# Kernel optimization log

Hardware: AMD Instinct MI355X
Metric: run time of the kernel (lower is better)

The kernel has to match this reference:

```python
import jax, jax.numpy as jnp
import numpy as np

N = 100000
E = 1600000
D_IN = 256
HID = 128
EPS = 1e-5


def setup_inputs() -> dict:
    key = jax.random.key(0)
    ks = jax.random.split(key, 8)
    x = jax.random.normal(ks[0], (N, D_IN), dtype=jnp.float32)
    edge_index = jax.random.randint(ks[1], (2, E), 0, N, dtype=jnp.int64)
    edge_weight = jax.random.uniform(ks[2], (E,), dtype=jnp.float32)
    # GCNConv lin weights (glorot-ish scale) + bias
    W1 = jax.random.normal(ks[3], (D_IN, HID), dtype=jnp.float32) / np.sqrt(D_IN)
    b1 = jnp.zeros((HID,), dtype=jnp.float32)
    W2 = jax.random.normal(ks[4], (HID, HID), dtype=jnp.float32) / np.sqrt(HID)
    b2 = jnp.zeros((HID,), dtype=jnp.float32)
    # BatchNorm affine params
    g1 = jnp.ones((HID,), dtype=jnp.float32)
    be1 = jnp.zeros((HID,), dtype=jnp.float32)
    g2 = jnp.ones((HID,), dtype=jnp.float32)
    be2 = jnp.zeros((HID,), dtype=jnp.float32)
    return {"x": x, "edge_index": edge_index, "edge_weight": edge_weight,
            "W1": W1, "b1": b1, "g1": g1, "be1": be1,
            "W2": W2, "b2": b2, "g2": g2, "be2": be2}


def _gcn_layer(h, src, dst, w, W, b):
    # GCNConv(add_self_loops=False, normalize=False):
    # h' = h @ W; out[i] = sum_{(j->i)} w_ji * h'[j]; out += b
    h = h @ W                                   # [N, out_dim]
    msg = w[:, None] * jnp.take(h, src, axis=0)  # [E, out_dim]
    agg = jax.ops.segment_sum(msg, dst, num_segments=N)
    return agg + b


def _bn(h, gamma, beta):
    # BatchNorm1d with batch statistics (biased variance), training-mode math
    mean = jnp.mean(h, axis=0)
    var = jnp.mean(jnp.square(h - mean), axis=0)
    return (h - mean) * jax.lax.rsqrt(var + EPS) * gamma + beta


def reference(x, edge_index, edge_weight, W1, b1, g1, be1, W2, b2, g2, be2):
    src = edge_index[0]
    dst = edge_index[1]
    h = _gcn_layer(x, src, dst, edge_weight, W1, b1)
    h = jax.nn.relu(_bn(h, g1, be1))
    h = _gcn_layer(h, src, dst, edge_weight, W2, b2)
    h = jax.nn.relu(_bn(h, g2, be2))  # last_activation=True
    return h
```

## Files before the change

### kernel.cpp

```cpp
#include <hip/hip_runtime.h>
#include <hip/hip_bf16.h>

#define NNODES 100000
#define DIN    256
#define NHID   128
#define EPS    1e-5f
#define SHIFT  9
#define NB2    ((NNODES + 511) >> SHIFT)
#define BCAP2  9216
#define CURPAD 16
#define PH     2048

typedef __attribute__((ext_vector_type(8))) short short8v;
typedef __attribute__((ext_vector_type(4))) float f32x4;

static __device__ __forceinline__ unsigned short f2bf(float v) {
    __hip_bfloat16 b = __float2bfloat16(v);
    return *reinterpret_cast<unsigned short*>(&b);
}
static __device__ __forceinline__ float bfhi2f(unsigned int u) {
    union { unsigned int i; float f; } x; x.i = u & 0xFFFF0000u; return x.f;
}
static __device__ __forceinline__ float bflo2f(unsigned int u) {
    union { unsigned int i; float f; } x; x.i = u << 16; return x.f;
}

__global__ __launch_bounds__(256) void wtrans2_kernel(const float* __restrict__ W1,
                                                      const float* __restrict__ W2,
                                                      unsigned short* __restrict__ Wt1,
                                                      unsigned short* __restrict__ Wt2) {
    int i = blockIdx.x * 256 + threadIdx.x;
    if (i < DIN * NHID) {
        const int k = i >> 7, c = i & 127;
        Wt1[c * DIN + k] = f2bf(W1[i]);
    } else {
        i -= DIN * NHID;
        if (i < NHID * NHID) {
            const int k = i >> 7, c = i & 127;
            Wt2[c * NHID + k] = f2bf(W2[i]);
        }
    }
}

template <int K, int MODE>
__global__ __launch_bounds__(256) void mfma_gemm(const float* __restrict__ Af,
                                                 const unsigned short* __restrict__ Wtb,
                                                 const float* __restrict__ SS,
                                                 unsigned short* __restrict__ C, int M) {
    constexpr int NS = K / 32;
    constexpr int PADB = 40;
    __shared__ unsigned short As[2][128 * PADB];
    __shared__ float ssl[256];

    const int t = threadIdx.x;
    if (MODE == 1) {
        ssl[t] = SS[t];
        __syncthreads();
    }

    const int wid = t >> 6;
    const int lane = t & 63;
    const int wr = wid >> 1, wc = wid & 1;
    const int l15 = lane & 15, g = lane >> 4;
    const int R0 = blockIdx.x * 128;
    const int RW = R0 + wr * 64;

    const int srow = t >> 3;
    const int scol = (t & 7) * 4;

    f32x4 acc[4][4] = {};

    auto STAGE = [&](int s, int buf) {
        const int k0 = s * 32;
#pragma unroll
        for (int i = 0; i < 4; ++i) {
            const int row = srow + i * 32;
            int grow = R0 + row;
            grow = grow < M ? grow : M - 1;
            float4 v = *reinterpret_cast<const float4*>(Af + (size_t)grow * K + k0 + scol);
            if (MODE == 1) {
                v.x = fmaxf(fmaf(v.x, ssl[k0 + scol],     ssl[128 + k0 + scol]),     0.f);
                v.y = fmaxf(fmaf(v.y, ssl[k0 + scol + 1], ssl[128 + k0 + scol + 1]), 0.f);
                v.z = fmaxf(fmaf(v.z, ssl[k0 + scol + 2], ssl[128 + k0 + scol + 2]), 0.f);
                v.w = fmaxf(fmaf(v.w, ssl[k0 + scol + 3], ssl[128 + k0 + scol + 3]), 0.f);
            }
            ushort4 bv;
            bv.x = f2bf(v.x); bv.y = f2bf(v.y); bv.z = f2bf(v.z); bv.w = f2bf(v.w);
            *reinterpret_cast<ushort4*>(&As[buf][row * PADB + scol]) = bv;
        }
    };

    STAGE(0, 0);
    __syncthreads();

    for (int s = 0; s < NS; ++s) {
        if (s + 1 < NS) STAGE(s + 1, (s + 1) & 1);
        const unsigned short* ab = As[s & 1];
        short8v b[4];
#pragma unroll
        for (int n = 0; n < 4; ++n) {
            const int col = wc * 64 + n * 16 + l15;
            b[n] = *reinterpret_cast<const short8v*>(&Wtb[(size_t)col * K + s * 32 + g * 8]);
        }
        short8v a[4];
#pragma unroll
        for (int m = 0; m < 4; ++m) {
            const int row = wr * 64 + m * 16 + l15;
            a[m] = *reinterpret_cast<const short8v*>(&ab[row * PADB + g * 8]);
        }
#pragma unroll
        for (int m = 0; m < 4; ++m)
#pragma unroll
            for (int n = 0; n < 4; ++n)
                acc[m][n] = __builtin_amdgcn_mfma_f32_16x16x32_bf16(a[m], b[n], acc[m][n], 0, 0, 0);
        __syncthreads();
    }

#pragma unroll
    for (int m = 0; m < 4; ++m) {
#pragma unroll
        for (int q = 0; q < 4; ++q) {
            const int row = RW + m * 16 + g * 4 + q;
            if (row < M) {
                unsigned short* cp = C + (size_t)row * NHID + wc * 64 + l15;
#pragma unroll
                for (int n = 0; n < 4; ++n)
                    cp[n * 16] = f2bf(acc[m][n][q]);
            }
        }
    }
}

__global__ __launch_bounds__(256) void part_kernel(const int* __restrict__ src,
                                                   const int* __restrict__ dst,
                                                   const float* __restrict__ w,
                                                   int* __restrict__ gcur,
                                                   int2* __restrict__ bstage, int E) {
    __shared__ int2 staged[PH];
    __shared__ unsigned char aux[PH];
    __shared__ int hist[NB2], scn[NB2], cur[NB2], gbase[NB2];
    __shared__ int part[256];

    const int t = threadIdx.x;
    const int nchunk = (E + PH - 1) / PH;
    for (int c = blockIdx.x; c < nchunk; c += gridDim.x) {
        const int e0 = c * PH;
        const int cnt = min(PH, E - e0);
        for (int i = t; i < NB2; i += 256) hist[i] = 0;
        __syncthreads();

        int2 pay[8];
        int bk[8];
#pragma unroll
        for (int j = 0; j < 8; ++j) {
            const int i = j * 256 + t;
            bk[j] = -1;
            if (i < cnt) {
                const int e = e0 + i;
                const int d = dst[e];
                bk[j] = d >> SHIFT;
                pay[j].x = src[e] | ((d & 511) << 17);
                pay[j].y = __float_as_int(w[e]);
                atomicAdd(&hist[bk[j]], 1);
            }
        }
        __syncthreads();

        part[t] = (t < NB2) ? hist[t] : 0;
        __syncthreads();
        for (int off = 1; off < 256; off <<= 1) {
            const int v = (t >= off) ? part[t - off] : 0;
            __syncthreads();
            part[t] += v;
            __syncthreads();
        }
        if (t < NB2) {
            const int ex = part[t] - hist[t];
            scn[t] = ex;
            cur[t] = ex;
        }
        __syncthreads();

#pragma unroll
        for (int j = 0; j < 8; ++j) {
            if (bk[j] >= 0) {
                const int p = atomicAdd(&cur[bk[j]], 1);
                staged[p] = pay[j];
                aux[p] = (unsigned char)bk[j];
            }
        }
        if (t < NB2 && hist[t] > 0) gbase[t] = atomicAdd(&gcur[t * CURPAD], hist[t]);
        __syncthreads();

        for (int i = t; i < cnt; i += 256) {
            const int b = aux[i];
            const int p = gbase[b] + (i - scn[b]);
            if (p < BCAP2) bstage[(size_t)b * BCAP2 + p] = staged[i];
        }
        __syncthreads();
    }
}

__global__ __launch_bounds__(256) void csr_kernel(const int* __restrict__ gcur,
                                                  const int2* __restrict__ bstage,
                                                  int2* __restrict__ row_be,
                                                  int2* __restrict__ s_iw) {
    const int b = blockIdx.x;
    const int t = threadIdx.x;
    int cnt = gcur[b * CURPAD];
    if (cnt > BCAP2) cnt = BCAP2;
    const int sbase = b * BCAP2;

    __shared__ int hist[512], cur[512];
    __shared__ int part[256];
    for (int i = t; i < 512; i += 256) hist[i] = 0;
    __syncthreads();
    for (int i = t; i < cnt; i += 256)
        atomicAdd(&hist[(bstage[sbase + i].x >> 17) & 511], 1);
    __syncthreads();

    int loc[2];
    loc[0] = hist[t * 2];
    loc[1] = hist[t * 2 + 1];
    const int s0 = loc[0] + loc[1];
    part[t] = s0;
    __syncthreads();
    for (int off = 1; off < 256; off <<= 1) {
        const int v = (t >= off) ? part[t - off] : 0;
        __syncthreads();
        part[t] += v;
        __syncthreads();
    }
    int run = part[t] - s0;
#pragma unroll
    for (int j = 0; j < 2; ++j) {
        const int lb = t * 2 + j;
        cur[lb] = run;
        const int d = (b << SHIFT) + lb;
        if (d < NNODES) {
            int2 be;
            be.x = sbase + run;
            be.y = sbase + run + loc[j];
            row_be[d] = be;
        }
        run += loc[j];
    }
    __syncthreads();

    for (int i = t; i < cnt; i += 256) {
        const int2 e = bstage[sbase + i];
        const int l = (e.x >> 17) & 511;
        const int p = atomicAdd(&cur[l], 1);
        int2 o;
        o.x = e.x & 0x1FFFF;
        o.y = e.y;
        s_iw[sbase + p] = o;
    }
}

__global__ __launch_bounds__(256) void aggregate_kernel(const unsigned short* __restrict__ hb,
                                                        const int2* __restrict__ row_be,
                                                        const int2* __restrict__ s_iw,
                                                        float* __restrict__ out, int n) {
    const int wid = (blockIdx.x * 256 + threadIdx.x) >> 6;
    if (wid >= n) return;
    const int lane = threadIdx.x & 63;
    const int grp = lane >> 4;
    const int l16 = lane & 15;
    const int2 be = row_be[wid];
    const int end = be.y;

    float acc[8] = {};
    int j = be.x + grp;
    for (; j + 4 < end; j += 8) {
        const int2 e0 = s_iw[j];
        const int2 e1 = s_iw[j + 4];
        const uint4 v0 = *reinterpret_cast<const uint4*>(hb + (size_t)e0.x * NHID + l16 * 8);
        const uint4 v1 = *reinterpret_cast<const uint4*>(hb + (size_t)e1.x * NHID + l16 * 8);
        const float w0 = __int_as_float(e0.y);
        const float w1 = __int_as_float(e1.y);
        acc[0] = fmaf(w0, bflo2f(v0.x), acc[0]); acc[1] = fmaf(w0, bfhi2f(v0.x), acc[1]);
        acc[2] = fmaf(w0, bflo2f(v0.y), acc[2]); acc[3] = fmaf(w0, bfhi2f(v0.y), acc[3]);
        acc[4] = fmaf(w0, bflo2f(v0.z), acc[4]); acc[5] = fmaf(w0, bfhi2f(v0.z), acc[5]);
        acc[6] = fmaf(w0, bflo2f(v0.w), acc[6]); acc[7] = fmaf(w0, bfhi2f(v0.w), acc[7]);
        acc[0] = fmaf(w1, bflo2f(v1.x), acc[0]); acc[1] = fmaf(w1, bfhi2f(v1.x), acc[1]);
        acc[2] = fmaf(w1, bflo2f(v1.y), acc[2]); acc[3] = fmaf(w1, bfhi2f(v1.y), acc[3]);
        acc[4] = fmaf(w1, bflo2f(v1.z), acc[4]); acc[5] = fmaf(w1, bfhi2f(v1.z), acc[5]);
        acc[6] = fmaf(w1, bflo2f(v1.w), acc[6]); acc[7] = fmaf(w1, bfhi2f(v1.w), acc[7]);
    }
    if (j < end) {
        const int2 e0 = s_iw[j];
        const uint4 v0 = *reinterpret_cast<const uint4*>(hb + (size_t)e0.x * NHID + l16 * 8);
        const float w0 = __int_as_float(e0.y);
        acc[0] = fmaf(w0, bflo2f(v0.x), acc[0]); acc[1] = fmaf(w0, bfhi2f(v0.x), acc[1]);
        acc[2] = fmaf(w0, bflo2f(v0.y), acc[2]); acc[3] = fmaf(w0, bfhi2f(v0.y), acc[3]);
        acc[4] = fmaf(w0, bflo2f(v0.z), acc[4]); acc[5] = fmaf(w0, bfhi2f(v0.z), acc[5]);
        acc[6] = fmaf(w0, bflo2f(v0.w), acc[6]); acc[7] = fmaf(w0, bfhi2f(v0.w), acc[7]);
    }
#pragma unroll
    for (int k = 0; k < 8; ++k) {
        acc[k] += __shfl_xor(acc[k], 16, 64);
        acc[k] += __shfl_xor(acc[k], 32, 64);
    }
    if (grp == 0) {
        float4 a, b;
        a.x = acc[0]; a.y = acc[1]; a.z = acc[2]; a.w = acc[3];
        b.x = acc[4]; b.y = acc[5]; b.z = acc[6]; b.w = acc[7];
        float4* op = reinterpret_cast<float4*>(out + (size_t)wid * NHID + l16 * 8);
        op[0] = a;
        op[1] = b;
    }
}

__global__ __launch_bounds__(256) void stats_kernel(const float* __restrict__ h,
                                                    float* __restrict__ sums, int nrows) {
    const int col = threadIdx.x & 127;
    const int half = threadIdx.x >> 7;
    float s = 0.f, sq = 0.f;
    for (int r = blockIdx.x * 2 + half; r < nrows; r += gridDim.x * 2) {
        const float v = h[(size_t)r * NHID + col];
        s += v;
        sq += v * v;
    }
    __shared__ float ls[256], lq[256];
    ls[threadIdx.x] = s;
    lq[threadIdx.x] = sq;
    __syncthreads();
    if (threadIdx.x < 128) {
        atomicAdd(&sums[col], ls[threadIdx.x] + ls[threadIdx.x + 128]);
        atomicAdd(&sums[128 + col], lq[threadIdx.x] + lq[threadIdx.x + 128]);
    }
}

__global__ void finalize_kernel(const float* __restrict__ sums,
                                const float* __restrict__ gamma,
                                const float* __restrict__ beta,
                                float* __restrict__ ss) {
    const int c = threadIdx.x;
    const float invN = 1.0f / (float)NNODES;
    const float mean = sums[c] * invN;
    const float var = sums[128 + c] * invN - mean * mean;
    const float scale = gamma[c] * rsqrtf(var + EPS);
    ss[c] = scale;
    ss[128 + c] = beta[c] - mean * scale;
}

__global__ __launch_bounds__(256) void apply_f32_kernel(const float* __restrict__ in,
                                                        const float* __restrict__ ss,
                                                        float* __restrict__ out, int n4) {
    const int idx = blockIdx.x * 256 + threadIdx.x;
    if (idx >= n4) return;
    const int c = (idx & 31) * 4;
    const float4 v = reinterpret_cast<const float4*>(in)[idx];
    const float4 sc = *reinterpret_cast<const float4*>(ss + c);
    const float4 sh = *reinterpret_cast<const float4*>(ss + 128 + c);
    float4 r;
    r.x = fmaxf(fmaf(v.x, sc.x, sh.x), 0.f);
    r.y = fmaxf(fmaf(v.y, sc.y, sh.y), 0.f);
    r.z = fmaxf(fmaf(v.z, sc.z, sh.z), 0.f);
    r.w = fmaxf(fmaf(v.w, sc.w, sh.w), 0.f);
    reinterpret_cast<float4*>(out)[idx] = r;
}

extern "C" void kernel_launch(void* const* d_in, const int* in_sizes, int n_in,
                              void* d_out, int out_size, void* d_ws, size_t ws_size,
                              hipStream_t stream) {
    const float* x   = (const float*)d_in[0];
    const int*   ei  = (const int*)d_in[1];
    const float* ew  = (const float*)d_in[2];
    const float* W1  = (const float*)d_in[3];
    const float* g1  = (const float*)d_in[5];
    const float* be1 = (const float*)d_in[6];
    const float* W2  = (const float*)d_in[7];
    const float* g2  = (const float*)d_in[9];
    const float* be2 = (const float*)d_in[10];
    float* out = (float*)d_out;

    const int M = NNODES;
    const int E = in_sizes[2];
    const int* src = ei;
    const int* dst = ei + E;

    unsigned short* hb = (unsigned short*)d_ws;
    float* agg   = (float*)(hb + (size_t)M * NHID);
    int2* bstage = (int2*)(agg + (size_t)M * NHID);
    int2* s_iw   = bstage + (size_t)NB2 * BCAP2;
    int2* row_be = s_iw + (size_t)NB2 * BCAP2;
    int* gcur    = (int*)(row_be + NNODES);
    unsigned short* Wt1b = (unsigned short*)(gcur + NB2 * CURPAD);
    unsigned short* Wt2b = Wt1b + DIN * NHID;
    float* sums  = (float*)(Wt2b + NHID * NHID);
    float* ss    = sums + 512;

    const int gemm_grid = (M + 127) / 128;
    const int n4 = M * NHID / 4;
    const int app_grid = (n4 + 255) / 256;
    const int agg_grid = (M * 64 + 255) / 256;
    const int part_grid = (E + PH - 1) / PH;

    wtrans2_kernel<<<(DIN * NHID + NHID * NHID + 255) / 256, 256, 0, stream>>>(W1, W2, Wt1b, Wt2b);
    hipMemsetAsync(gcur, 0, (size_t)NB2 * CURPAD * sizeof(int), stream);
    hipMemsetAsync(sums, 0, 512 * sizeof(float), stream);
    part_kernel<<<part_grid, 256, 0, stream>>>(src, dst, ew, gcur, bstage, E);
    csr_kernel<<<NB2, 256, 0, stream>>>(gcur, bstage, row_be, s_iw);

    mfma_gemm<DIN, 0><<<gemm_grid, 256, 0, stream>>>(x, Wt1b, nullptr, hb, M);
    aggregate_kernel<<<agg_grid, 256, 0, stream>>>(hb, row_be, s_iw, agg, M);
    stats_kernel<<<1024, 256, 0, stream>>>(agg, sums, M);
    finalize_kernel<<<1, 128, 0, stream>>>(sums, g1, be1, ss);

    mfma_gemm<NHID, 1><<<gemm_grid, 256, 0, stream>>>(agg, Wt2b, ss, hb, M);
    aggregate_kernel<<<agg_grid, 256, 0, stream>>>(hb, row_be, s_iw, agg, M);
    stats_kernel<<<1024, 256, 0, stream>>>(agg, sums + 256, M);
    finalize_kernel<<<1, 128, 0, stream>>>(sums + 256, g2, be2, ss);
    apply_f32_kernel<<<app_grid, 256, 0, stream>>>(agg, ss, out, n4);
}
```

Before: 344.7 us.

## Fuse BatchNorm stats into persistent aggregate kernel and merge setup memsets

The aggregate kernel becomes a grid-stride persistent kernel that also accumulates per-column sum and sum-of-squares in registers and reduces them through shared memory and atomics. This removes the separate stats kernels, which re-read the whole aggregated matrix. The gather loop is unrolled to four edges per group for more memory-level parallelism. The weight-transpose kernel now also zeroes the counters and sums in place of two memsets, and the CSR build uses 512 threads so each thread handles one bucket. The risks are higher register pressure from the unroll and extra accumulators, and load imbalance across the fixed-size persistent grid.

```diff
diff --git a/kernel.cpp b/kernel.cpp
--- a/kernel.cpp
+++ b/kernel.cpp
@@ -10,6 +10,7 @@
 #define BCAP2  9216
 #define CURPAD 16
 #define PH     2048
+#define AGGBLK 2048
 
 typedef __attribute__((ext_vector_type(8))) short short8v;
 typedef __attribute__((ext_vector_type(4))) float f32x4;
@@ -25,21 +26,28 @@
     union { unsigned int i; float f; } x; x.i = u << 16; return x.f;
 }
 
-__global__ __launch_bounds__(256) void wtrans2_kernel(const float* __restrict__ W1,
-                                                      const float* __restrict__ W2,
-                                                      unsigned short* __restrict__ Wt1,
-                                                      unsigned short* __restrict__ Wt2) {
+__global__ __launch_bounds__(256) void prep_kernel(const float* __restrict__ W1,
+                                                   const float* __restrict__ W2,
+                                                   unsigned short* __restrict__ Wt1,
+                                                   unsigned short* __restrict__ Wt2,
+                                                   int* __restrict__ gcur,
+                                                   float* __restrict__ sums) {
     int i = blockIdx.x * 256 + threadIdx.x;
     if (i < DIN * NHID) {
         const int k = i >> 7, c = i & 127;
         Wt1[c * DIN + k] = f2bf(W1[i]);
-    } else {
-        i -= DIN * NHID;
-        if (i < NHID * NHID) {
-            const int k = i >> 7, c = i & 127;
-            Wt2[c * NHID + k] = f2bf(W2[i]);
-        }
-    }
+        return;
+    }
+    i -= DIN * NHID;
+    if (i < NHID * NHID) {
+        const int k = i >> 7, c = i & 127;
+        Wt2[c * NHID + k] = f2bf(W2[i]);
+        return;
+    }
+    i -= NHID * NHID;
+    if (i < NB2 * CURPAD) { gcur[i] = 0; return; }
+    i -= NB2 * CURPAD;
+    if (i < 512) sums[i] = 0.f;
 }
 
 template <int K, int MODE>
@@ -201,7 +209,7 @@
     }
 }
 
-__global__ __launch_bounds__(256) void csr_kernel(const int* __restrict__ gcur,
+__global__ __launch_bounds__(512) void csr_kernel(const int* __restrict__ gcur,
                                                   const int2* __restrict__ bstage,
                                                   int2* __restrict__ row_be,
                                                   int2* __restrict__ s_iw) {
@@ -212,42 +220,33 @@
     const int sbase = b * BCAP2;
 
     __shared__ int hist[512], cur[512];
-    __shared__ int part[256];
-    for (int i = t; i < 512; i += 256) hist[i] = 0;
-    __syncthreads();
-    for (int i = t; i < cnt; i += 256)
+    __shared__ int part[512];
+    hist[t] = 0;
+    __syncthreads();
+    for (int i = t; i < cnt; i += 512)
         atomicAdd(&hist[(bstage[sbase + i].x >> 17) & 511], 1);
     __syncthreads();
 
-    int loc[2];
-    loc[0] = hist[t * 2];
-    loc[1] = hist[t * 2 + 1];
-    const int s0 = loc[0] + loc[1];
-    part[t] = s0;
-    __syncthreads();
-    for (int off = 1; off < 256; off <<= 1) {
+    part[t] = hist[t];
+    __syncthreads();
+    for (int off = 1; off < 512; off <<= 1) {
         const int v = (t >= off) ? part[t - off] : 0;
         __syncthreads();
         part[t] += v;
         __syncthreads();
     }
-    int run = part[t] - s0;
-#pragma unroll
-    for (int j = 0; j < 2; ++j) {
-        const int lb = t * 2 + j;
-        cur[lb] = run;
-        const int d = (b << SHIFT) + lb;
-        if (d < NNODES) {
-            int2 be;
-            be.x = sbase + run;
-            be.y = sbase + run + loc[j];
-            row_be[d] = be;
-        }
-        run += loc[j];
-    }
-    __syncthreads();
-
-    for (int i = t; i < cnt; i += 256) {
+    const int excl = part[t] - hist[t];
+    cur[t] = excl;
+    const int d = (b << SHIFT) + t;
+    if (d < NNODES) {
+        int2 be;
+        be.x = sbase + excl;
+        be.y = sbase + part[t];
+        row_be[d] = be;
+    }
+    __syncthreads();
+
+    for (int i = t; i < cnt; i += 512) {
         const int2 e = bstage[sbase + i];
         const int l = (e.x >> 17) & 511;
         const int p = atomicAdd(&cur[l], 1);
@@ -258,77 +257,95 @@
     }
 }
 
+#define EDGE_FMA(eN, vN)                                                        \
+    {                                                                           \
+        const float wN = __int_as_float(eN.y);                                  \
+        acc[0] = fmaf(wN, bflo2f(vN.x), acc[0]);                                \
+        acc[1] = fmaf(wN, bfhi2f(vN.x), acc[1]);                                \
+        acc[2] = fmaf(wN, bflo2f(vN.y), acc[2]);                                \
+        acc[3] = fmaf(wN, bfhi2f(vN.y), acc[3]);                                \
+        acc[4] = fmaf(wN, bflo2f(vN.z), acc[4]);                                \
+        acc[5] = fmaf(wN, bfhi2f(vN.z), acc[5]);                                \
+        acc[6] = fmaf(wN, bflo2f(vN.w), acc[6]);                                \
+        acc[7] = fmaf(wN, bfhi2f(vN.w), acc[7]);                                \
+    }
+
 __global__ __launch_bounds__(256) void aggregate_kernel(const unsigned short* __restrict__ hb,
                                                         const int2* __restrict__ row_be,
                                                         const int2* __restrict__ s_iw,
-                                                        float* __restrict__ out, int n) {
-    const int wid = (blockIdx.x * 256 + threadIdx.x) >> 6;
-    if (wid >= n) return;
-    const int lane = threadIdx.x & 63;
+                                                        float* __restrict__ out,
+                                                        float* __restrict__ sums, int n) {
+    const int t = threadIdx.x;
+    const int lane = t & 63;
     const int grp = lane >> 4;
     const int l16 = lane & 15;
-    const int2 be = row_be[wid];
-    const int end = be.y;
-
-    float acc[8] = {};
-    int j = be.x + grp;
-    for (; j + 4 < end; j += 8) {
-        const int2 e0 = s_iw[j];
-        const int2 e1 = s_iw[j + 4];
-        const uint4 v0 = *reinterpret_cast<const uint4*>(hb + (size_t)e0.x * NHID + l16 * 8);
-        const uint4 v1 = *reinterpret_cast<const uint4*>(hb + (size_t)e1.x * NHID + l16 * 8);
-        const float w0 = __int_as_float(e0.y);
-        const float w1 = __int_as_float(e1.y);
-        acc[0] = fmaf(w0, bflo2f(v0.x), acc[0]); acc[1] = fmaf(w0, bfhi2f(v0.x), acc[1]);
-        acc[2] = fmaf(w0, bflo2f(v0.y), acc[2]); acc[3] = fmaf(w0, bfhi2f(v0.y), acc[3]);
-        acc[4] = fmaf(w0, bflo2f(v0.z), acc[4]); acc[5] = fmaf(w0, bfhi2f(v0.z), acc[5]);
-        acc[6] = fmaf(w0, bflo2f(v0.w), acc[6]); acc[7] = fmaf(w0, bfhi2f(v0.w), acc[7]);
-        acc[0] = fmaf(w1, bflo2f(v1.x), acc[0]); acc[1] = fmaf(w1, bfhi2f(v1.x), acc[1]);
-        acc[2] = fmaf(w1, bflo2f(v1.y), acc[2]); acc[3] = fmaf(w1, bfhi2f(v1.y), acc[3]);
-        acc[4] = fmaf(w1, bflo2f(v1.z), acc[4]); acc[5] = fmaf(w1, bfhi2f(v1.z), acc[5]);
-        acc[6] = fmaf(w1, bflo2f(v1.w), acc[6]); acc[7] = fmaf(w1, bfhi2f(v1.w), acc[7]);
-    }
-    if (j < end) {
-        const int2 e0 = s_iw[j];
-        const uint4 v0 = *reinterpret_cast<const uint4*>(hb + (size_t)e0.x * NHID + l16 * 8);
-        const float w0 = __int_as_float(e0.y);
-        acc[0] = fmaf(w0, bflo2f(v0.x), acc[0]); acc[1] = fmaf(w0, bfhi2f(v0.x), acc[1]);
-        acc[2] = fmaf(w0, bflo2f(v0.y), acc[2]); acc[3] = fmaf(w0, bfhi2f(v0.y), acc[3]);
-        acc[4] = fmaf(w0, bflo2f(v0.z), acc[4]); acc[5] = fmaf(w0, bfhi2f(v0.z), acc[5]);
-        acc[6] = fmaf(w0, bflo2f(v0.w), acc[6]); acc[7] = fmaf(w0, bfhi2f(v0.w), acc[7]);
-    }
-#pragma unroll
-    for (int k = 0; k < 8; ++k) {
-        acc[k] += __shfl_xor(acc[k], 16, 64);
-        acc[k] += __shfl_xor(acc[k], 32, 64);
-    }
+    const int wav = t >> 6;
+    const int wid0 = (blockIdx.x * 256 + t) >> 6;
+    const int wstride = (AGGBLK * 256) >> 6;
+
+    float s_acc[8] = {};
+    float q_acc[8] = {};
+
+    for (int wid = wid0; wid < n; wid += wstride) {
+        const int2 be = row_be[wid];
+        const int end = be.y;
+        float acc[8] = {};
+        int j = be.x + grp;
+        for (; j + 12 < end; j += 16) {
+            const int2 e0 = s_iw[j];
+            const int2 e1 = s_iw[j + 4];
+            const int2 e2 = s_iw[j + 8];
+            const int2 e3 = s_iw[j + 12];
+            const uint4 v0 = *reinterpret_cast<const uint4*>(hb + (size_t)e0.x * NHID + l16 * 8);
+            const uint4 v1 = *reinterpret_cast<const uint4*>(hb + (size_t)e1.x * NHID + l16 * 8);
+            const uint4 v2 = *reinterpret_cast<const uint4*>(hb + (size_t)e2.x * NHID + l16 * 8);
+            const uint4 v3 = *reinterpret_cast<const uint4*>(hb + (size_t)e3.x * NHID + l16 * 8);
+            EDGE_FMA(e0, v0);
+            EDGE_FMA(e1, v1);
+            EDGE_FMA(e2, v2);
+            EDGE_FMA(e3, v3);
+        }
+        for (; j < end; j += 4) {
+            const int2 e0 = s_iw[j];
+            const uint4 v0 = *reinterpret_cast<const uint4*>(hb + (size_t)e0.x * NHID + l16 * 8);
+            EDGE_FMA(e0, v0);
+        }
+#pragma unroll
+        for (int k = 0; k < 8; ++k) {
+            acc[k] += __shfl_xor(acc[k], 16, 64);
+            acc[k] += __shfl_xor(acc[k], 32, 64);
+        }
+        if (grp == 0) {
+            float4 a, b;
+            a.x = acc[0]; a.y = acc[1]; a.z = acc[2]; a.w = acc[3];
+            b.x = acc[4]; b.y = acc[5]; b.z = acc[6]; b.w = acc[7];
+            float4* op = reinterpret_cast<float4*>(out + (size_t)wid * NHID + l16 * 8);
+            op[0] = a;
+            op[1] = b;
+#pragma unroll
+            for (int k = 0; k < 8; ++k) {
+                s_acc[k] += acc[k];
+                q_acc[k] = fmaf(acc[k], acc[k], q_acc[k]);
+            }
+        }
+    }
+
+    __shared__ float ls[4][128], lq[4][128];
     if (grp == 0) {
-        float4 a, b;
-        a.x = acc[0]; a.y = acc[1]; a.z = acc[2]; a.w = acc[3];
-        b.x = acc[4]; b.y = acc[5]; b.z = acc[6]; b.w = acc[7];
-        float4* op = reinterpret_cast<float4*>(out + (size_t)wid * NHID + l16 * 8);
-        op[0] = a;
-        op[1] = b;
-    }
-}
-
-__global__ __launch_bounds__(256) void stats_kernel(const float* __restrict__ h,
-                                                    float* __restrict__ sums, int nrows) {
-    const int col = threadIdx.x & 127;
-    const int half = threadIdx.x >> 7;
-    float s = 0.f, sq = 0.f;
-    for (int r = blockIdx.x * 2 + half; r < nrows; r += gridDim.x * 2) {
-        const float v = h[(size_t)r * NHID + col];
-        s += v;
-        sq += v * v;
-    }
-    __shared__ float ls[256], lq[256];
-    ls[threadIdx.x] = s;
-    lq[threadIdx.x] = sq;
-    __syncthreads();
-    if (threadIdx.x < 128) {
-        atomicAdd(&sums[col], ls[threadIdx.x] + ls[threadIdx.x + 128]);
-        atomicAdd(&sums[128 + col], lq[threadIdx.x] + lq[threadIdx.x + 128]);
+#pragma unroll
+        for (int k = 0; k < 8; ++k) {
+            ls[wav][l16 * 8 + k] = s_acc[k];
+            lq[wav][l16 * 8 + k] = q_acc[k];
+        }
+    }
+    __syncthreads();
+    if (t < 128) {
+        const float v = ls[0][t] + ls[1][t] + ls[2][t] + ls[3][t];
+        atomicAdd(&sums[t], v);
+    } else {
+        const int c = t - 128;
+        const float v = lq[0][c] + lq[1][c] + lq[2][c] + lq[3][c];
+        atomicAdd(&sums[128 + c], v);
     }
 }
 
@@ -395,23 +412,19 @@
     const int gemm_grid = (M + 127) / 128;
     const int n4 = M * NHID / 4;
     const int app_grid = (n4 + 255) / 256;
-    const int agg_grid = (M * 64 + 255) / 256;
     const int part_grid = (E + PH - 1) / PH;
-
-    wtrans2_kernel<<<(DIN * NHID + NHID * NHID + 255) / 256, 256, 0, stream>>>(W1, W2, Wt1b, Wt2b);
-    hipMemsetAsync(gcur, 0, (size_t)NB2 * CURPAD * sizeof(int), stream);
-    hipMemsetAsync(sums, 0, 512 * sizeof(float), stream);
+    const int prep_tot = DIN * NHID + NHID * NHID + NB2 * CURPAD + 512;
+
+    prep_kernel<<<(prep_tot + 255) / 256, 256, 0, stream>>>(W1, W2, Wt1b, Wt2b, gcur, sums);
     part_kernel<<<part_grid, 256, 0, stream>>>(src, dst, ew, gcur, bstage, E);
-    csr_kernel<<<NB2, 256, 0, stream>>>(gcur, bstage, row_be, s_iw);
+    csr_kernel<<<NB2, 512, 0, stream>>>(gcur, bstage, row_be, s_iw);
 
     mfma_gemm<DIN, 0><<<gemm_grid, 256, 0, stream>>>(x, Wt1b, nullptr, hb, M);
-    aggregate_kernel<<<agg_grid, 256, 0, stream>>>(hb, row_be, s_iw, agg, M);
-    stats_kernel<<<1024, 256, 0, stream>>>(agg, sums, M);
+    aggregate_kernel<<<AGGBLK, 256, 0, stream>>>(hb, row_be, s_iw, agg, sums, M);
     finalize_kernel<<<1, 128, 0, stream>>>(sums, g1, be1, ss);
 
     mfma_gemm<NHID, 1><<<gemm_grid, 256, 0, stream>>>(agg, Wt2b, ss, hb, M);
-    aggregate_kernel<<<agg_grid, 256, 0, stream>>>(hb, row_be, s_iw, agg, M);
-    stats_kernel<<<1024, 256, 0, stream>>>(agg, sums + 256, M);
+    aggregate_kernel<<<AGGBLK, 256, 0, stream>>>(hb, row_be, s_iw, agg, sums + 256, M);
     finalize_kernel<<<1, 128, 0, stream>>>(sums + 256, g2, be2, ss);
     apply_f32_kernel<<<app_grid, 256, 0, stream>>>(agg, ss, out, n4);
 }
```

Result: slower. 355.3 us (+3.0%).
